# Performance work log

Measured on AMD Instinct MI355X. Metric: run time of the kernel, lower is better.

The kernel has to match this reference:

```python
import jax, jax.numpy as jnp
import numpy as np

N = 100000   # nodes
E = 3200000  # edges (avg degree 32)
D = 128      # in_channels
H = 128      # hidden_channels
A, S, ETH = 3, 2, 3  # head output dims


def _w(k, o, i):
    return jax.random.normal(k, (o, i), dtype=jnp.float32) / np.sqrt(i).astype(np.float32)


def setup_inputs() -> dict:
    key = jax.random.key(0)
    ks = jax.random.split(key, 20)
    x = jax.random.normal(ks[0], (N, D), dtype=jnp.float32)
    edge_index = jax.random.randint(ks[1], (2, E), 0, N, dtype=jnp.int64)
    inp = {"x": x, "edge_index": edge_index}
    # SAGEConv params: Wl applied to mean-aggregated neighbors, Wr to root, plus bias
    dims = [("1", D, H), ("2", H, H), ("3", H, H), ("a", H, A), ("s", H, S), ("e", H, ETH)]
    ki = 2
    for tag, i, o in dims:
        inp[f"W{tag}l"] = _w(ks[ki], o, i); ki += 1
        inp[f"W{tag}r"] = _w(ks[ki], o, i); ki += 1
        inp[f"b{tag}"] = jnp.zeros((o,), dtype=jnp.float32)
    return inp


def _sage(x, src, dst, inv_deg, Wl, Wr, b):
    # mean aggregation of source features onto destination nodes, then linear
    agg = jax.ops.segment_sum(x[src], dst, num_segments=N) * inv_deg  # [N, d]
    return agg @ Wl.T + x @ Wr.T + b


def reference(x, edge_index,
              W1l, W1r, b1, W2l, W2r, b2, W3l, W3r, b3,
              Wal, War, ba, Wsl, Wsr, bs, Wel, Wer, be):
    src, dst = edge_index[0], edge_index[1]
    deg = jax.ops.segment_sum(jnp.ones((E,), jnp.float32), dst, num_segments=N)
    inv_deg = (1.0 / jnp.maximum(deg, 1.0))[:, None]  # [N,1]
    h = jax.nn.relu(_sage(x, src, dst, inv_deg, W1l, W1r, b1))
    h = jax.nn.relu(_sage(h, src, dst, inv_deg, W2l, W2r, b2))
    h = jax.nn.relu(_sage(h, src, dst, inv_deg, W3l, W3r, b3))
    age_out = _sage(h, src, dst, inv_deg, Wal, War, ba)
    sex_out = _sage(h, src, dst, inv_deg, Wsl, Wsr, bs)
    eth_out = _sage(h, src, dst, inv_deg, Wel, Wer, be)
    return (age_out, sex_out, eth_out)
```

## Files before the change

kernel.cpp:

```cpp
#include <hip/hip_runtime.h>

#define TPB 256
#define NB1 256
#define NBUCK 512

using half4_t = __attribute__((ext_vector_type(4))) _Float16;
using half8_t = __attribute__((ext_vector_type(8))) _Float16;
using f32x4 = __attribute__((ext_vector_type(4))) float;


__global__ __launch_bounds__(256) void hist1_k(const int* __restrict__ ei,
                                               int* __restrict__ hist, int E, int stripe) {
  __shared__ int h[NBUCK];
  for (int i = threadIdx.x; i < NBUCK; i += 256) h[i] = 0;
  __syncthreads();
  int b0 = blockIdx.x * stripe;
  int b1 = min(b0 + stripe, E);
  for (int e = b0 + threadIdx.x; e < b1; e += 256) atomicAdd(&h[ei[E + e] >> 8], 1);
  __syncthreads();
  for (int i = threadIdx.x; i < NBUCK; i += 256) hist[i * NB1 + blockIdx.x] = h[i];
}

__global__ void scan1_k(const int* __restrict__ src, int* __restrict__ out,
                        int* __restrict__ chunk, int n) {
  __shared__ int sh[TPB];
  int i = blockIdx.x * TPB + threadIdx.x;
  int v = (i < n) ? src[i] : 0;
  sh[threadIdx.x] = v;
  __syncthreads();
  for (int off = 1; off < TPB; off <<= 1) {
    int t = (threadIdx.x >= off) ? sh[threadIdx.x - off] : 0;
    __syncthreads();
    sh[threadIdx.x] += t;
    __syncthreads();
  }
  if (i < n) out[i] = sh[threadIdx.x] - v;
  if (threadIdx.x == TPB - 1) chunk[blockIdx.x] = sh[TPB - 1];
}

__global__ void scan2_k(int* __restrict__ chunk, int nb) {
  __shared__ int sh[512];
  int v = (threadIdx.x < nb) ? chunk[threadIdx.x] : 0;
  sh[threadIdx.x] = v;
  __syncthreads();
  for (int off = 1; off < 512; off <<= 1) {
    int t = (threadIdx.x >= off) ? sh[threadIdx.x - off] : 0;
    __syncthreads();
    sh[threadIdx.x] += t;
    __syncthreads();
  }
  if (threadIdx.x < nb) chunk[threadIdx.x] = sh[threadIdx.x] - v;
}

__global__ void scan3_k(int* __restrict__ out, const int* __restrict__ chunk, int n) {
  int i = blockIdx.x * TPB + threadIdx.x;
  if (i < n) out[i] += chunk[blockIdx.x];
}

__global__ __launch_bounds__(256) void scatter1_k(const int* __restrict__ ei,
                                                  const int* __restrict__ base,
                                                  unsigned* __restrict__ ebuf, int E,
                                                  int stripe) {
  __shared__ int cur[NBUCK];
  for (int i = threadIdx.x; i < NBUCK; i += 256) cur[i] = base[i * NB1 + blockIdx.x];
  __syncthreads();
  int b0 = blockIdx.x * stripe;
  int b1 = min(b0 + stripe, E);
  for (int e = b0 + threadIdx.x; e < b1; e += 256) {
    int s = ei[e];
    int d = ei[E + e];
    int p = atomicAdd(&cur[d >> 8], 1);
    ebuf[p] = (unsigned)s | ((unsigned)(d & 255) << 24);
  }
}

__global__ __launch_bounds__(256) void build_k(const unsigned* __restrict__ ebuf,
                                               const int* __restrict__ base,
                                               int* __restrict__ row_start,
                                               int* __restrict__ deg,
                                               float* __restrict__ invd,
                                               int* __restrict__ csr, int N, int E) {
  __shared__ int h[256];
  __shared__ int excl[256];
  __shared__ int bse[2];
  int b = blockIdx.x;
  int t = threadIdx.x;
  if (t == 0) {
    bse[0] = base[b * NB1];
    bse[1] = (b + 1 < NBUCK) ? base[(b + 1) * NB1] : E;
  }
  h[t] = 0;
  __syncthreads();
  int bs = bse[0], be = bse[1];
  for (int e = bs + t; e < be; e += 256) atomicAdd(&h[ebuf[e] >> 24], 1);
  __syncthreads();
  int v = h[t];
  excl[t] = v;
  __syncthreads();
  for (int off = 1; off < 256; off <<= 1) {
    int tv = (t >= off) ? excl[t - off] : 0;
    __syncthreads();
    excl[t] += tv;
    __syncthreads();
  }
  int ex = excl[t] - v;
  int node = b * 256 + t;
  if (node < N) {
    row_start[node] = bs + ex;
    deg[node] = v;
    invd[node] = 1.0f / fmaxf((float)v, 1.0f);
  }
  h[t] = bs + ex;
  __syncthreads();
  for (int e = bs + t; e < be; e += 256) {
    unsigned p = ebuf[e];
    int pos = atomicAdd(&h[p >> 24], 1);
    csr[pos] = (int)(p & 0xFFFFFFu);
  }
}


__global__ void f2h_k(const float* __restrict__ in, _Float16* __restrict__ out, int n4) {
  int i = blockIdx.x * TPB + threadIdx.x;
  if (i < n4) {
    float4 v = ((const float4*)in)[i];
    half4_t o;
    o.x = (_Float16)v.x; o.y = (_Float16)v.y; o.z = (_Float16)v.z; o.w = (_Float16)v.w;
    ((half4_t*)out)[i] = o;
  }
}

__global__ void w6_k(const float* __restrict__ w0, const float* __restrict__ w1,
                     const float* __restrict__ w2, const float* __restrict__ w3,
                     const float* __restrict__ w4, const float* __restrict__ w5,
                     _Float16* __restrict__ out) {
  int t = blockIdx.x * TPB + threadIdx.x;
  if (t >= 6 * 4096) return;
  int which = t >> 12, i = t & 4095;
  const float* src = which == 0 ? w0 : which == 1 ? w1 : which == 2 ? w2
                   : which == 3 ? w3 : which == 4 ? w4 : w5;
  float4 v = ((const float4*)src)[i];
  half4_t o;
  o.x = (_Float16)v.x; o.y = (_Float16)v.y; o.z = (_Float16)v.z; o.w = (_Float16)v.w;
  ((half4_t*)out)[(size_t)which * 4096 + i] = o;
}


__global__ __launch_bounds__(256) void agg128_k(const _Float16* __restrict__ hb,
                                                const int* __restrict__ csr,
                                                const int* __restrict__ row_start,
                                                const int* __restrict__ deg,
                                                const float* __restrict__ invd,
                                                _Float16* __restrict__ out, int n) {
  int node = (blockIdx.x << 2) + (threadIdx.x >> 6);
  if (node >= n) return;
  int lane = threadIdx.x & 63;
  int g = lane >> 4;
  int l = lane & 15;
  int s = row_start[node];
  int c = deg[node];
  const _Float16* base = hb + (l << 3);
  float a0 = 0.f, a1 = 0.f, a2 = 0.f, a3 = 0.f;
  float a4 = 0.f, a5 = 0.f, a6 = 0.f, a7 = 0.f;
  int j = 0;
  if (c >= 16) {
    int id[4];
#pragma unroll
    for (int p = 0; p < 4; ++p) id[p] = csr[s + 4 * p + g];
    while (true) {
      half8_t v[4];
#pragma unroll
      for (int p = 0; p < 4; ++p) v[p] = *(const half8_t*)&base[(size_t)id[p] * 128];
      j += 16;
      bool more = (j + 16 <= c);
      if (more) {
#pragma unroll
        for (int p = 0; p < 4; ++p) id[p] = csr[s + j + 4 * p + g];
      }
#pragma unroll
      for (int p = 0; p < 4; ++p) {
        a0 += (float)v[p][0]; a1 += (float)v[p][1];
        a2 += (float)v[p][2]; a3 += (float)v[p][3];
        a4 += (float)v[p][4]; a5 += (float)v[p][5];
        a6 += (float)v[p][6]; a7 += (float)v[p][7];
      }
      if (!more) break;
    }
  }
  if (j < c) {
    int cm1 = c - 1;
#pragma unroll
    for (int p = 0; p < 4; ++p) {
      int e = j + 4 * p + g;
      float m = (e < c) ? 1.f : 0.f;
      int id = csr[s + min(e, cm1)];
      half8_t v = *(const half8_t*)&base[(size_t)id * 128];
      a0 = fmaf(m, (float)v[0], a0); a1 = fmaf(m, (float)v[1], a1);
      a2 = fmaf(m, (float)v[2], a2); a3 = fmaf(m, (float)v[3], a3);
      a4 = fmaf(m, (float)v[4], a4); a5 = fmaf(m, (float)v[5], a5);
      a6 = fmaf(m, (float)v[6], a6); a7 = fmaf(m, (float)v[7], a7);
    }
  }
  a0 += __shfl_xor(a0, 16); a1 += __shfl_xor(a1, 16);
  a2 += __shfl_xor(a2, 16); a3 += __shfl_xor(a3, 16);
  a4 += __shfl_xor(a4, 16); a5 += __shfl_xor(a5, 16);
  a6 += __shfl_xor(a6, 16); a7 += __shfl_xor(a7, 16);
  a0 += __shfl_xor(a0, 32); a1 += __shfl_xor(a1, 32);
  a2 += __shfl_xor(a2, 32); a3 += __shfl_xor(a3, 32);
  a4 += __shfl_xor(a4, 32); a5 += __shfl_xor(a5, 32);
  a6 += __shfl_xor(a6, 32); a7 += __shfl_xor(a7, 32);
  if (g == 0) {
    float w = invd[node];
    half8_t r;
    r[0] = (_Float16)(a0 * w); r[1] = (_Float16)(a1 * w);
    r[2] = (_Float16)(a2 * w); r[3] = (_Float16)(a3 * w);
    r[4] = (_Float16)(a4 * w); r[5] = (_Float16)(a5 * w);
    r[6] = (_Float16)(a6 * w); r[7] = (_Float16)(a7 * w);
    *(half8_t*)&out[(size_t)node * 128 + (l << 3)] = r;
  }
}


__global__ __launch_bounds__(256) void gemm2_k(
    const _Float16* __restrict__ Aagg, const _Float16* __restrict__ Ah,
    const _Float16* __restrict__ Wh,
    const float* __restrict__ bias, _Float16* __restrict__ outh, int n, int do_relu) {
  int wave = threadIdx.x >> 6;
  int lane = threadIdx.x & 63;
  int quad = lane >> 4;
  int l16 = lane & 15;
  int m0 = blockIdx.x * 64 + wave * 16;
  int arow = m0 + l16;
  bool valid = arow < n;
  size_t abase = (size_t)arow * 128 + quad * 8;

  f32x4 acc[8];
#pragma unroll
  for (int c = 0; c < 8; ++c) acc[c] = (f32x4){0.f, 0.f, 0.f, 0.f};

#pragma unroll
  for (int s = 0; s < 2; ++s) {
    const _Float16* A = s ? Ah : Aagg;
    const _Float16* W = Wh + (size_t)s * 16384;
#pragma unroll
    for (int kb = 0; kb < 128; kb += 32) {
      half8_t af;
      if (valid) {
        af = *(const half8_t*)&A[abase + kb];
      } else {
#pragma unroll
        for (int jj = 0; jj < 8; ++jj) af[jj] = (_Float16)0;
      }
#pragma unroll
      for (int c = 0; c < 8; ++c) {
        half8_t bf = *(const half8_t*)&W[(size_t)(c * 16 + l16) * 128 + kb + quad * 8];
        acc[c] = __builtin_amdgcn_mfma_f32_16x16x32_f16(af, bf, acc[c], 0, 0, 0);
      }
    }
  }

#pragma unroll
  for (int c = 0; c < 8; ++c) {
    float bcol = bias[c * 16 + l16];
#pragma unroll
    for (int r = 0; r < 4; ++r) {
      int row = m0 + quad * 4 + r;
      if (row < n) {
        float v = acc[c][r] + bcol;
        if (do_relu) v = fmaxf(v, 0.f);
        outh[(size_t)row * 128 + c * 16 + l16] = (_Float16)v;
      }
    }
  }
}


__global__ void pack_head_k(const float* __restrict__ Wal, const float* __restrict__ War,
                            const float* __restrict__ ba, const float* __restrict__ Wsl,
                            const float* __restrict__ Wsr, const float* __restrict__ bsx,
                            const float* __restrict__ Wel, const float* __restrict__ Wer,
                            const float* __restrict__ be, _Float16* __restrict__ Wcat,
                            float* __restrict__ bcat) {
  int t = blockIdx.x * TPB + threadIdx.x;
  float v = 0.f;
  bool ok = t < 2048;
  if (t < 384) v = Wal[t];
  else if (t < 640) v = Wsl[t - 384];
  else if (t < 1024) v = Wel[t - 640];
  else if (t < 1408) v = War[t - 1024];
  else if (t < 1664) v = Wsr[t - 1408];
  else if (t < 2048) v = Wer[t - 1664];
  if (ok) Wcat[t] = (_Float16)v;
  if (t < 16) {
    float b = 0.f;
    if (t >= 8 && t < 11) b = ba[t - 8];
    else if (t >= 11 && t < 13) b = bsx[t - 11];
    else if (t >= 13) b = be[t - 13];
    bcat[t] = b;
  }
}


__global__ __launch_bounds__(256) void head_gemm_k(const _Float16* __restrict__ h,
                                                   const _Float16* __restrict__ Wcat,
                                                   const float* __restrict__ bcat,
                                                   float* __restrict__ out_lr, int n) {
  __shared__ float hs[64 * 132];
  __shared__ float Ws[16 * 128];
  __shared__ float bsh[16];
  int tid = threadIdx.x;
  int m0 = blockIdx.x * 64;
  {
    half8_t w = *(const half8_t*)&Wcat[tid * 8];
#pragma unroll
    for (int jj = 0; jj < 8; ++jj) Ws[tid * 8 + jj] = (float)w[jj];
    if (tid < 16) bsh[tid] = bcat[tid];
  }
  {
    int row = tid >> 2, q = tid & 3;
    int grow = m0 + row;
#pragma unroll
    for (int j = 0; j < 4; ++j) {
      half8_t v;
      if (grow < n) {
        v = *(const half8_t*)&h[(size_t)grow * 128 + q * 32 + j * 8];
      } else {
#pragma unroll
        for (int jj = 0; jj < 8; ++jj) v[jj] = (_Float16)0;
      }
#pragma unroll
      for (int jj = 0; jj < 8; ++jj) hs[row * 132 + q * 32 + j * 8 + jj] = (float)v[jj];
    }
  }
  __syncthreads();
  int row = tid & 63, og = tid >> 6;
  float acc[4] = {0.f, 0.f, 0.f, 0.f};
#pragma unroll
  for (int k4 = 0; k4 < 32; ++k4) {
    float4 hv = *(float4*)&hs[row * 132 + k4 * 4];
#pragma unroll
    for (int i = 0; i < 4; ++i) {
      float4 wv = *(float4*)&Ws[(og * 4 + i) * 128 + k4 * 4];
      acc[i] += hv.x * wv.x + hv.y * wv.y + hv.z * wv.z + hv.w * wv.w;
    }
  }
  int grow = m0 + row;
  if (grow < n) {
#pragma unroll
    for (int i = 0; i < 4; ++i)
      out_lr[(size_t)grow * 16 + og * 4 + i] = acc[i] + bsh[og * 4 + i];
  }
}


__global__ void agg8_k(const float* __restrict__ hlr, const int* __restrict__ csr,
                       const int* __restrict__ row_start, const int* __restrict__ deg,
                       const float* __restrict__ invd, float* __restrict__ out, int n) {
  int node = (blockIdx.x << 2) + (threadIdx.x >> 6);
  if (node >= n) return;
  int lane = threadIdx.x & 63;
  int c2 = lane & 3;
  int g = lane >> 2;
  int s = row_start[node], cnt = deg[node];
  float ax = 0.f, ay = 0.f;
  int j = 0;
  for (; j + 32 <= cnt; j += 32) {
#pragma unroll
    for (int p = 0; p < 2; ++p) {
      int id = csr[s + j + 16 * p + g];
      float2 v = *(const float2*)&hlr[(size_t)id * 16 + 2 * c2];
      ax += v.x;
      ay += v.y;
    }
  }
  if (j < cnt) {
    int cm1 = cnt - 1;
#pragma unroll
    for (int p = 0; p < 2; ++p) {
      int e = j + 16 * p + g;
      float m = (e < cnt) ? 1.f : 0.f;
      int id = csr[s + min(e, cm1)];
      float2 v = *(const float2*)&hlr[(size_t)id * 16 + 2 * c2];
      ax = fmaf(m, v.x, ax);
      ay = fmaf(m, v.y, ay);
    }
  }
  ax += __shfl_xor(ax, 4);  ay += __shfl_xor(ay, 4);
  ax += __shfl_xor(ax, 8);  ay += __shfl_xor(ay, 8);
  ax += __shfl_xor(ax, 16); ay += __shfl_xor(ay, 16);
  ax += __shfl_xor(ax, 32); ay += __shfl_xor(ay, 32);
  if (g == 0) {
    float w = invd[node];
    float r0 = ax * w + hlr[(size_t)node * 16 + 8 + 2 * c2];
    float r1 = ay * w + hlr[(size_t)node * 16 + 8 + 2 * c2 + 1];
    float rr[2] = {r0, r1};
#pragma unroll
    for (int q = 0; q < 2; ++q) {
      int f = 2 * c2 + q;
      float r = rr[q];
      if (f < 3) out[(size_t)node * 3 + f] = r;
      else if (f < 5) out[(size_t)3 * n + (size_t)node * 2 + (f - 3)] = r;
      else out[(size_t)5 * n + (size_t)node * 3 + (f - 5)] = r;
    }
  }
}


extern "C" void kernel_launch(void* const* d_in, const int* in_sizes, int n_in,
                              void* d_out, int out_size, void* d_ws, size_t ws_size,
                              hipStream_t stream) {
  const float* x = (const float*)d_in[0];
  const int* ei = (const int*)d_in[1];
  const float* W1l = (const float*)d_in[2];
  const float* W1r = (const float*)d_in[3];
  const float* b1 = (const float*)d_in[4];
  const float* W2l = (const float*)d_in[5];
  const float* W2r = (const float*)d_in[6];
  const float* b2 = (const float*)d_in[7];
  const float* W3l = (const float*)d_in[8];
  const float* W3r = (const float*)d_in[9];
  const float* b3 = (const float*)d_in[10];
  const float* Wal = (const float*)d_in[11];
  const float* War = (const float*)d_in[12];
  const float* ba = (const float*)d_in[13];
  const float* Wsl = (const float*)d_in[14];
  const float* Wsr = (const float*)d_in[15];
  const float* bsx = (const float*)d_in[16];
  const float* Wel = (const float*)d_in[17];
  const float* Wer = (const float*)d_in[18];
  const float* be = (const float*)d_in[19];

  int N = in_sizes[0] / 128;
  int E = in_sizes[1] / 2;
  int NBKT = (N + 255) >> 8;

  char* w = (char*)d_ws;
  auto alloc = [&](size_t b) {
    char* p = w;
    w += (b + 255) & ~(size_t)255;
    return p;
  };
  int* deg = (int*)alloc((size_t)N * 4);
  int* row_start = (int*)alloc((size_t)N * 4);
  float* invd = (float*)alloc((size_t)N * 4);
  int* hist = (int*)alloc((size_t)NBUCK * NB1 * 4);
  int* chunk = (int*)alloc(512 * 4);
  int* csr = (int*)alloc((size_t)E * 4);
  size_t xh_bytes = (size_t)N * 128 * 2;
  size_t ebuf_bytes = (size_t)E * 4;
  char* region = (char*)alloc(xh_bytes > ebuf_bytes ? xh_bytes : ebuf_bytes);
  unsigned* ebuf = (unsigned*)region;
  _Float16* xh = (_Float16*)region;
  _Float16* aggh = (_Float16*)alloc((size_t)N * 128 * 2);
  _Float16* hA = (_Float16*)alloc((size_t)N * 128 * 2);
  _Float16* hB = (_Float16*)alloc((size_t)N * 128 * 2);
  _Float16* wh = (_Float16*)alloc((size_t)6 * 16384 * 2);
  _Float16* Wcat = (_Float16*)alloc(2048 * 2);
  float* bcat = (float*)alloc(16 * 4);
  float* head_lr = (float*)alloc((size_t)N * 16 * 4);

  int stripe = (((E + NB1 - 1) / NB1) + 255) & ~255;
  int nscan = NBUCK * NB1;
  int nbScan = (nscan + TPB - 1) / TPB;
  int nbNode = (N + 3) / 4;
  int nbM = (N + 63) / 64;
  int nbC = (N * 32 + TPB - 1) / TPB;

  hist1_k<<<NB1, 256, 0, stream>>>(ei, hist, E, stripe);
  scan1_k<<<nbScan, TPB, 0, stream>>>(hist, hist, chunk, nscan);
  scan2_k<<<1, 512, 0, stream>>>(chunk, nbScan);
  scan3_k<<<nbScan, TPB, 0, stream>>>(hist, chunk, nscan);
  scatter1_k<<<NB1, 256, 0, stream>>>(ei, hist, ebuf, E, stripe);
  build_k<<<NBKT, 256, 0, stream>>>(ebuf, hist, row_start, deg, invd, csr, N, E);

  f2h_k<<<nbC, TPB, 0, stream>>>(x, xh, N * 32);
  w6_k<<<96, TPB, 0, stream>>>(W1l, W1r, W2l, W2r, W3l, W3r, wh);
  pack_head_k<<<8, TPB, 0, stream>>>(Wal, War, ba, Wsl, Wsr, bsx, Wel, Wer, be, Wcat, bcat);

  agg128_k<<<nbNode, TPB, 0, stream>>>(xh, csr, row_start, deg, invd, aggh, N);
  gemm2_k<<<nbM, TPB, 0, stream>>>(aggh, xh, wh + 0 * 16384, b1, hA, N, 1);
  agg128_k<<<nbNode, TPB, 0, stream>>>(hA, csr, row_start, deg, invd, aggh, N);
  gemm2_k<<<nbM, TPB, 0, stream>>>(aggh, hA, wh + 2 * 16384, b2, hB, N, 1);
  agg128_k<<<nbNode, TPB, 0, stream>>>(hB, csr, row_start, deg, invd, aggh, N);
  gemm2_k<<<nbM, TPB, 0, stream>>>(aggh, hB, wh + 4 * 16384, b3, hA, N, 1);
  head_gemm_k<<<nbM, TPB, 0, stream>>>(hA, Wcat, bcat, head_lr, N);
  agg8_k<<<nbNode, TPB, 0, stream>>>(head_lr, csr, row_start, deg, invd, (float*)d_out, N);
}
```

Baseline: 798.8 us.

## Fuse neighbor aggregation, SAGE GEMM and head projection into one kernel

Replaces separate agg128/gemm2/head_gemm kernels with a fused kernel where each wave aggregates 16 nodes into LDS, then runs MFMA GEMM directly from LDS. The last layer also applies the head projection from LDS, skipping the hA write and reread. This removes the intermediate aggregation buffer traffic and kernel launches. In exchange, each wave now processes 16 nodes serially with far fewer blocks, which may reduce gather parallelism.

```diff
diff --git a/kernel.cpp b/kernel.cpp
--- a/kernel.cpp
+++ b/kernel.cpp
@@ -143,135 +143,6 @@
   half4_t o;
   o.x = (_Float16)v.x; o.y = (_Float16)v.y; o.z = (_Float16)v.z; o.w = (_Float16)v.w;
   ((half4_t*)out)[(size_t)which * 4096 + i] = o;
-}
-
-
-__global__ __launch_bounds__(256) void agg128_k(const _Float16* __restrict__ hb,
-                                                const int* __restrict__ csr,
-                                                const int* __restrict__ row_start,
-                                                const int* __restrict__ deg,
-                                                const float* __restrict__ invd,
-                                                _Float16* __restrict__ out, int n) {
-  int node = (blockIdx.x << 2) + (threadIdx.x >> 6);
-  if (node >= n) return;
-  int lane = threadIdx.x & 63;
-  int g = lane >> 4;
-  int l = lane & 15;
-  int s = row_start[node];
-  int c = deg[node];
-  const _Float16* base = hb + (l << 3);
-  float a0 = 0.f, a1 = 0.f, a2 = 0.f, a3 = 0.f;
-  float a4 = 0.f, a5 = 0.f, a6 = 0.f, a7 = 0.f;
-  int j = 0;
-  if (c >= 16) {
-    int id[4];
-#pragma unroll
-    for (int p = 0; p < 4; ++p) id[p] = csr[s + 4 * p + g];
-    while (true) {
-      half8_t v[4];
-#pragma unroll
-      for (int p = 0; p < 4; ++p) v[p] = *(const half8_t*)&base[(size_t)id[p] * 128];
-      j += 16;
-      bool more = (j + 16 <= c);
-      if (more) {
-#pragma unroll
-        for (int p = 0; p < 4; ++p) id[p] = csr[s + j + 4 * p + g];
-      }
-#pragma unroll
-      for (int p = 0; p < 4; ++p) {
-        a0 += (float)v[p][0]; a1 += (float)v[p][1];
-        a2 += (float)v[p][2]; a3 += (float)v[p][3];
-        a4 += (float)v[p][4]; a5 += (float)v[p][5];
-        a6 += (float)v[p][6]; a7 += (float)v[p][7];
-      }
-      if (!more) break;
-    }
-  }
-  if (j < c) {
-    int cm1 = c - 1;
-#pragma unroll
-    for (int p = 0; p < 4; ++p) {
-      int e = j + 4 * p + g;
-      float m = (e < c) ? 1.f : 0.f;
-      int id = csr[s + min(e, cm1)];
-      half8_t v = *(const half8_t*)&base[(size_t)id * 128];
-      a0 = fmaf(m, (float)v[0], a0); a1 = fmaf(m, (float)v[1], a1);
-      a2 = fmaf(m, (float)v[2], a2); a3 = fmaf(m, (float)v[3], a3);
-      a4 = fmaf(m, (float)v[4], a4); a5 = fmaf(m, (float)v[5], a5);
-      a6 = fmaf(m, (float)v[6], a6); a7 = fmaf(m, (float)v[7], a7);
-    }
-  }
-  a0 += __shfl_xor(a0, 16); a1 += __shfl_xor(a1, 16);
-  a2 += __shfl_xor(a2, 16); a3 += __shfl_xor(a3, 16);
-  a4 += __shfl_xor(a4, 16); a5 += __shfl_xor(a5, 16);
-  a6 += __shfl_xor(a6, 16); a7 += __shfl_xor(a7, 16);
-  a0 += __shfl_xor(a0, 32); a1 += __shfl_xor(a1, 32);
-  a2 += __shfl_xor(a2, 32); a3 += __shfl_xor(a3, 32);
-  a4 += __shfl_xor(a4, 32); a5 += __shfl_xor(a5, 32);
-  a6 += __shfl_xor(a6, 32); a7 += __shfl_xor(a7, 32);
-  if (g == 0) {
-    float w = invd[node];
-    half8_t r;
-    r[0] = (_Float16)(a0 * w); r[1] = (_Float16)(a1 * w);
-    r[2] = (_Float16)(a2 * w); r[3] = (_Float16)(a3 * w);
-    r[4] = (_Float16)(a4 * w); r[5] = (_Float16)(a5 * w);
-    r[6] = (_Float16)(a6 * w); r[7] = (_Float16)(a7 * w);
-    *(half8_t*)&out[(size_t)node * 128 + (l << 3)] = r;
-  }
-}
-
-
-__global__ __launch_bounds__(256) void gemm2_k(
-    const _Float16* __restrict__ Aagg, const _Float16* __restrict__ Ah,
-    const _Float16* __restrict__ Wh,
-    const float* __restrict__ bias, _Float16* __restrict__ outh, int n, int do_relu) {
-  int wave = threadIdx.x >> 6;
-  int lane = threadIdx.x & 63;
-  int quad = lane >> 4;
-  int l16 = lane & 15;
-  int m0 = blockIdx.x * 64 + wave * 16;
-  int arow = m0 + l16;
-  bool valid = arow < n;
-  size_t abase = (size_t)arow * 128 + quad * 8;
-
-  f32x4 acc[8];
-#pragma unroll
-  for (int c = 0; c < 8; ++c) acc[c] = (f32x4){0.f, 0.f, 0.f, 0.f};
-
-#pragma unroll
-  for (int s = 0; s < 2; ++s) {
-    const _Float16* A = s ? Ah : Aagg;
-    const _Float16* W = Wh + (size_t)s * 16384;
-#pragma unroll
-    for (int kb = 0; kb < 128; kb += 32) {
-      half8_t af;
-      if (valid) {
-        af = *(const half8_t*)&A[abase + kb];
-      } else {
-#pragma unroll
-        for (int jj = 0; jj < 8; ++jj) af[jj] = (_Float16)0;
-      }
-#pragma unroll
-      for (int c = 0; c < 8; ++c) {
-        half8_t bf = *(const half8_t*)&W[(size_t)(c * 16 + l16) * 128 + kb + quad * 8];
-        acc[c] = __builtin_amdgcn_mfma_f32_16x16x32_f16(af, bf, acc[c], 0, 0, 0);
-      }
-    }
-  }
-
-#pragma unroll
-  for (int c = 0; c < 8; ++c) {
-    float bcol = bias[c * 16 + l16];
-#pragma unroll
-    for (int r = 0; r < 4; ++r) {
-      int row = m0 + quad * 4 + r;
-      if (row < n) {
-        float v = acc[c][r] + bcol;
-        if (do_relu) v = fmaxf(v, 0.f);
-        outh[(size_t)row * 128 + c * 16 + l16] = (_Float16)v;
-      }
-    }
-  }
 }
 
 
@@ -301,54 +172,161 @@
 }
 
 
-__global__ __launch_bounds__(256) void head_gemm_k(const _Float16* __restrict__ h,
-                                                   const _Float16* __restrict__ Wcat,
-                                                   const float* __restrict__ bcat,
-                                                   float* __restrict__ out_lr, int n) {
-  __shared__ float hs[64 * 132];
-  __shared__ float Ws[16 * 128];
-  __shared__ float bsh[16];
-  int tid = threadIdx.x;
-  int m0 = blockIdx.x * 64;
+__global__ __launch_bounds__(256) void fused_sage_k(
+    const _Float16* __restrict__ hin, const _Float16* __restrict__ Wh,
+    const float* __restrict__ bias, const int* __restrict__ csr,
+    const int* __restrict__ row_start, const int* __restrict__ deg,
+    const float* __restrict__ invd, _Float16* __restrict__ hout,
+    const _Float16* __restrict__ Wcat, const float* __restrict__ bcat,
+    float* __restrict__ head_out, int n, int mode) {
+  __shared__ _Float16 At[64][144];
+  int wave = threadIdx.x >> 6;
+  int lane = threadIdx.x & 63;
+  int g = lane >> 4;
+  int l = lane & 15;
+  int ms = blockIdx.x * 64 + wave * 16;
+
+  const _Float16* gbase = hin + (l << 3);
+  for (int i = 0; i < 16; ++i) {
+    int node = ms + i;
+    float a0 = 0.f, a1 = 0.f, a2 = 0.f, a3 = 0.f;
+    float a4 = 0.f, a5 = 0.f, a6 = 0.f, a7 = 0.f;
+    if (node < n) {
+      int s = row_start[node];
+      int c = deg[node];
+      int j = 0;
+      if (c >= 16) {
+        int id[4];
+#pragma unroll
+        for (int p = 0; p < 4; ++p) id[p] = csr[s + 4 * p + g];
+        while (true) {
+          half8_t v[4];
+#pragma unroll
+          for (int p = 0; p < 4; ++p) v[p] = *(const half8_t*)&gbase[(size_t)id[p] * 128];
+          j += 16;
+          bool more = (j + 16 <= c);
+          if (more) {
+#pragma unroll
+            for (int p = 0; p < 4; ++p) id[p] = csr[s + j + 4 * p + g];
+          }
+#pragma unroll
+          for (int p = 0; p < 4; ++p) {
+            a0 += (float)v[p][0]; a1 += (float)v[p][1];
+            a2 += (float)v[p][2]; a3 += (float)v[p][3];
+            a4 += (float)v[p][4]; a5 += (float)v[p][5];
+            a6 += (float)v[p][6]; a7 += (float)v[p][7];
+          }
+          if (!more) break;
+        }
+      }
+      if (j < c) {
+        int cm1 = c - 1;
+#pragma unroll
+        for (int p = 0; p < 4; ++p) {
+          int e = j + 4 * p + g;
+          float m = (e < c) ? 1.f : 0.f;
+          int id = csr[s + min(e, cm1)];
+          half8_t v = *(const half8_t*)&gbase[(size_t)id * 128];
+          a0 = fmaf(m, (float)v[0], a0); a1 = fmaf(m, (float)v[1], a1);
+          a2 = fmaf(m, (float)v[2], a2); a3 = fmaf(m, (float)v[3], a3);
+          a4 = fmaf(m, (float)v[4], a4); a5 = fmaf(m, (float)v[5], a5);
+          a6 = fmaf(m, (float)v[6], a6); a7 = fmaf(m, (float)v[7], a7);
+        }
+      }
+    }
+    a0 += __shfl_xor(a0, 16); a1 += __shfl_xor(a1, 16);
+    a2 += __shfl_xor(a2, 16); a3 += __shfl_xor(a3, 16);
+    a4 += __shfl_xor(a4, 16); a5 += __shfl_xor(a5, 16);
+    a6 += __shfl_xor(a6, 16); a7 += __shfl_xor(a7, 16);
+    a0 += __shfl_xor(a0, 32); a1 += __shfl_xor(a1, 32);
+    a2 += __shfl_xor(a2, 32); a3 += __shfl_xor(a3, 32);
+    a4 += __shfl_xor(a4, 32); a5 += __shfl_xor(a5, 32);
+    a6 += __shfl_xor(a6, 32); a7 += __shfl_xor(a7, 32);
+    if (g == 0) {
+      float w = (node < n) ? invd[node] : 0.f;
+      half8_t r;
+      r[0] = (_Float16)(a0 * w); r[1] = (_Float16)(a1 * w);
+      r[2] = (_Float16)(a2 * w); r[3] = (_Float16)(a3 * w);
+      r[4] = (_Float16)(a4 * w); r[5] = (_Float16)(a5 * w);
+      r[6] = (_Float16)(a6 * w); r[7] = (_Float16)(a7 * w);
+      *(half8_t*)&At[wave * 16 + i][l << 3] = r;
+    }
+  }
+  __syncthreads();
+
+  int arow = ms + l;
+  bool valid = arow < n;
+  f32x4 acc[8];
+#pragma unroll
+  for (int c = 0; c < 8; ++c) acc[c] = (f32x4){0.f, 0.f, 0.f, 0.f};
+
+#pragma unroll
+  for (int kb = 0; kb < 128; kb += 32) {
+    half8_t af = *(const half8_t*)&At[wave * 16 + l][kb + g * 8];
+#pragma unroll
+    for (int c = 0; c < 8; ++c) {
+      half8_t bf = *(const half8_t*)&Wh[(size_t)(c * 16 + l) * 128 + kb + g * 8];
+      acc[c] = __builtin_amdgcn_mfma_f32_16x16x32_f16(af, bf, acc[c], 0, 0, 0);
+    }
+  }
   {
-    half8_t w = *(const half8_t*)&Wcat[tid * 8];
-#pragma unroll
-    for (int jj = 0; jj < 8; ++jj) Ws[tid * 8 + jj] = (float)w[jj];
-    if (tid < 16) bsh[tid] = bcat[tid];
-  }
-  {
-    int row = tid >> 2, q = tid & 3;
-    int grow = m0 + row;
-#pragma unroll
-    for (int j = 0; j < 4; ++j) {
-      half8_t v;
-      if (grow < n) {
-        v = *(const half8_t*)&h[(size_t)grow * 128 + q * 32 + j * 8];
+    const _Float16* W2 = Wh + 16384;
+    size_t abase = (size_t)arow * 128 + g * 8;
+#pragma unroll
+    for (int kb = 0; kb < 128; kb += 32) {
+      half8_t af;
+      if (valid) {
+        af = *(const half8_t*)&hin[abase + kb];
       } else {
 #pragma unroll
-        for (int jj = 0; jj < 8; ++jj) v[jj] = (_Float16)0;
-      }
-#pragma unroll
-      for (int jj = 0; jj < 8; ++jj) hs[row * 132 + q * 32 + j * 8 + jj] = (float)v[jj];
-    }
-  }
-  __syncthreads();
-  int row = tid & 63, og = tid >> 6;
-  float acc[4] = {0.f, 0.f, 0.f, 0.f};
-#pragma unroll
-  for (int k4 = 0; k4 < 32; ++k4) {
-    float4 hv = *(float4*)&hs[row * 132 + k4 * 4];
-#pragma unroll
-    for (int i = 0; i < 4; ++i) {
-      float4 wv = *(float4*)&Ws[(og * 4 + i) * 128 + k4 * 4];
-      acc[i] += hv.x * wv.x + hv.y * wv.y + hv.z * wv.z + hv.w * wv.w;
-    }
-  }
-  int grow = m0 + row;
-  if (grow < n) {
-#pragma unroll
-    for (int i = 0; i < 4; ++i)
-      out_lr[(size_t)grow * 16 + og * 4 + i] = acc[i] + bsh[og * 4 + i];
+        for (int jj = 0; jj < 8; ++jj) af[jj] = (_Float16)0;
+      }
+#pragma unroll
+      for (int c = 0; c < 8; ++c) {
+        half8_t bf = *(const half8_t*)&W2[(size_t)(c * 16 + l) * 128 + kb + g * 8];
+        acc[c] = __builtin_amdgcn_mfma_f32_16x16x32_f16(af, bf, acc[c], 0, 0, 0);
+      }
+    }
+  }
+
+  if (mode == 0) {
+#pragma unroll
+    for (int c = 0; c < 8; ++c) {
+      float bcol = bias[c * 16 + l];
+#pragma unroll
+      for (int r = 0; r < 4; ++r) {
+        int row = ms + g * 4 + r;
+        if (row < n) {
+          float v = fmaxf(acc[c][r] + bcol, 0.f);
+          hout[(size_t)row * 128 + c * 16 + l] = (_Float16)v;
+        }
+      }
+    }
+  } else {
+    __syncthreads();
+#pragma unroll
+    for (int c = 0; c < 8; ++c) {
+      float bcol = bias[c * 16 + l];
+#pragma unroll
+      for (int r = 0; r < 4; ++r) {
+        float v = fmaxf(acc[c][r] + bcol, 0.f);
+        At[wave * 16 + g * 4 + r][c * 16 + l] = (_Float16)v;
+      }
+    }
+    __syncthreads();
+    f32x4 ah = (f32x4){0.f, 0.f, 0.f, 0.f};
+#pragma unroll
+    for (int kb = 0; kb < 128; kb += 32) {
+      half8_t af = *(const half8_t*)&At[wave * 16 + l][kb + g * 8];
+      half8_t bf = *(const half8_t*)&Wcat[(size_t)l * 128 + kb + g * 8];
+      ah = __builtin_amdgcn_mfma_f32_16x16x32_f16(af, bf, ah, 0, 0, 0);
+    }
+    float bcol = bcat[l];
+#pragma unroll
+    for (int r = 0; r < 4; ++r) {
+      int row = ms + g * 4 + r;
+      if (row < n) head_out[(size_t)row * 16 + l] = ah[r] + bcol;
+    }
   }
 }
 
@@ -451,7 +429,6 @@
   char* region = (char*)alloc(xh_bytes > ebuf_bytes ? xh_bytes : ebuf_bytes);
   unsigned* ebuf = (unsigned*)region;
   _Float16* xh = (_Float16*)region;
-  _Float16* aggh = (_Float16*)alloc((size_t)N * 128 * 2);
   _Float16* hA = (_Float16*)alloc((size_t)N * 128 * 2);
   _Float16* hB = (_Float16*)alloc((size_t)N * 128 * 2);
   _Float16* wh = (_Float16*)alloc((size_t)6 * 16384 * 2);
@@ -477,12 +454,11 @@
   w6_k<<<96, TPB, 0, stream>>>(W1l, W1r, W2l, W2r, W3l, W3r, wh);
   pack_head_k<<<8, TPB, 0, stream>>>(Wal, War, ba, Wsl, Wsr, bsx, Wel, Wer, be, Wcat, bcat);
 
-  agg128_k<<<nbNode, TPB, 0, stream>>>(xh, csr, row_start, deg, invd, aggh, N);
-  gemm2_k<<<nbM, TPB, 0, stream>>>(aggh, xh, wh + 0 * 16384, b1, hA, N, 1);
-  agg128_k<<<nbNode, TPB, 0, stream>>>(hA, csr, row_start, deg, invd, aggh, N);
-  gemm2_k<<<nbM, TPB, 0, stream>>>(aggh, hA, wh + 2 * 16384, b2, hB, N, 1);
-  agg128_k<<<nbNode, TPB, 0, stream>>>(hB, csr, row_start, deg, invd, aggh, N);
-  gemm2_k<<<nbM, TPB, 0, stream>>>(aggh, hB, wh + 4 * 16384, b3, hA, N, 1);
-  head_gemm_k<<<nbM, TPB, 0, stream>>>(hA, Wcat, bcat, head_lr, N);
+  fused_sage_k<<<nbM, TPB, 0, stream>>>(xh, wh + 0 * 16384, b1, csr, row_start, deg,
+                                        invd, hA, nullptr, nullptr, nullptr, N, 0);
+  fused_sage_k<<<nbM, TPB, 0, stream>>>(hA, wh + 2 * 16384, b2, csr, row_start, deg,
+                                        invd, hB, nullptr, nullptr, nullptr, N, 0);
+  fused_sage_k<<<nbM, TPB, 0, stream>>>(hB, wh + 4 * 16384, b3, csr, row_start, deg,
+                                        invd, nullptr, Wcat, bcat, head_lr, N, 1);
   agg8_k<<<nbNode, TPB, 0, stream>>>(head_lr, csr, row_start, deg, invd, (float*)d_out, N);
 }
```

After: 782.3 us. 1.02x faster.
